# Performance work log

Measured on AMD Instinct MI355X. Metric: run time of the kernel, lower is better.

## Reference

```python
import jax, jax.numpy as jnp
import numpy as np

N, F_IN, F_OUT = 200000, 128, 64
H, DEG = 50000, 32            # num_hyperedges, nodes per hyperedge
E = H * DEG                   # total incidences


def setup_inputs() -> dict:
    key = jax.random.key(0)
    k1, k2, k3, k4 = jax.random.split(key, 4)
    x = jax.random.normal(k1, (N, F_IN), dtype=jnp.float32)
    W = jax.random.normal(k2, (F_OUT, F_IN), dtype=jnp.float32) / np.sqrt(F_IN)
    a = jax.random.normal(k3, (2 * F_OUT,), dtype=jnp.float32) / np.sqrt(2 * F_OUT)
    nodes = jax.random.randint(k4, (E,), 0, N, dtype=jnp.int32)
    edges = jnp.repeat(jnp.arange(H, dtype=jnp.int32), DEG)  # sorted edge ids, DEG nodes each
    hyperedge_index = jnp.stack([nodes, edges])  # (2, E)
    return {"x": x, "W": W, "a": a, "hyperedge_index": hyperedge_index}


def reference(x, W, a, hyperedge_index):
    # h = W x  (Linear without bias, weight stored as (out, in))
    h = x @ W.T                                   # (N, F_OUT)
    nodes = hyperedge_index[0]
    eid = hyperedge_index[1]                      # sorted, groups incidences per hyperedge

    # attention score for ordered pair (j,k): a[:F] . h_j + a[F:] . h_k
    s1 = h @ a[:F_OUT]                            # (N,) left-slot contribution per node
    s2 = h @ a[F_OUT:]                            # (N,) right-slot contribution per node
    s1e = s1[nodes]                               # (E,)
    s2e = s2[nodes]                               # (E,)

    counts = jax.ops.segment_sum(jnp.ones_like(eid), eid, num_segments=H)   # degree per edge
    starts = jnp.cumsum(counts) - counts
    rank = jnp.arange(E, dtype=eid.dtype) - starts[eid]                     # position within edge
    deg_e = counts[eid]
    # sum over pairs j<k of (s1_j + s2_k):
    #   node at rank r appears (deg-1-r) times in left slot, r times in right slot
    w1 = (deg_e - 1 - rank).astype(h.dtype)
    w2 = rank.astype(h.dtype)
    pair_sum = jax.ops.segment_sum(s1e * w1 + s2e * w2, eid, num_segments=H)
    npairs = (counts * (counts - 1)) // 2
    edge_attention = pair_sum / jnp.maximum(npairs, 1).astype(h.dtype)      # mean over pairs
    # all H edges have DEG>=2 nodes by construction, matching torch's non-empty filter
    return h, edge_attention
```

## Files before the change

kernel.cpp:

```cpp
#include <hip/hip_runtime.h>

#define F_IN  128
#define F_OUT 64
#define DEG   32

typedef __attribute__((ext_vector_type(8))) short  short8;
typedef __attribute__((ext_vector_type(4))) float  float4v;

__device__ __forceinline__ unsigned short f2bf(float f) {
    unsigned int u = __builtin_bit_cast(unsigned int, f);
    u += 0x7FFFu + ((u >> 16) & 1u);
    return (unsigned short)(u >> 16);
}

__device__ __forceinline__ short8 cvt8(float4v lo, float4v hi) {
    short8 r;
    r[0] = (short)f2bf(lo[0]); r[1] = (short)f2bf(lo[1]);
    r[2] = (short)f2bf(lo[2]); r[3] = (short)f2bf(lo[3]);
    r[4] = (short)f2bf(hi[0]); r[5] = (short)f2bf(hi[1]);
    r[6] = (short)f2bf(hi[2]); r[7] = (short)f2bf(hi[3]);
    return r;
}

__device__ __forceinline__ short8 load_cvt8(const float* __restrict__ p) {
    const float4v* q = (const float4v*)p;
    return cvt8(q[0], q[1]);
}

__global__ __launch_bounds__(256) void gemm_s12_kernel(
    const float* __restrict__ x, const float* __restrict__ W,
    const float* __restrict__ a, float* __restrict__ h_out,
    float2* __restrict__ s12, int N)
{
    __shared__ short8 wfrag[1024];

    const int tid = threadIdx.x;

#pragma unroll
    for (int i0 = 0; i0 < 1024; i0 += 256) {
        const int i     = i0 + tid;
        const int combo = i >> 6;
        const int sl    = i & 63;
        const int t  = combo >> 2;
        const int ks = combo & 3;
        const int n  = (sl & 15) + 16 * t;
        const int qq = sl >> 4;
        wfrag[i] = load_cvt8(W + n * F_IN + ks * 32 + qq * 8);
    }
    __syncthreads();

    const int lane = tid & 63;
    const int wave = tid >> 6;
    const int row_base = (blockIdx.x * 4 + wave) * 32;
    if (row_base >= N) return;

    const int m = lane & 15;
    const int q = lane >> 4;

    float a1v[4], a2v[4];
#pragma unroll
    for (int t = 0; t < 4; ++t) {
        a1v[t] = a[m + 16 * t];
        a2v[t] = a[F_OUT + m + 16 * t];
    }

#pragma unroll
    for (int s = 0; s < 2; ++s) {
        const int row0 = row_base + s * 16;
        const float* rowp = x + (size_t)(row0 + m) * F_IN + q * 8;

        float4v raw[4][2];
#pragma unroll
        for (int ks = 0; ks < 4; ++ks) {
            const float4v* p = (const float4v*)(rowp + ks * 32);
            raw[ks][0] = p[0];
            raw[ks][1] = p[1];
        }
        short8 afrag[4];
#pragma unroll
        for (int ks = 0; ks < 4; ++ks) afrag[ks] = cvt8(raw[ks][0], raw[ks][1]);

        float4v acc[4];
#pragma unroll
        for (int t = 0; t < 4; ++t) acc[t] = (float4v){0.f, 0.f, 0.f, 0.f};

#pragma unroll
        for (int ks = 0; ks < 4; ++ks) {
#pragma unroll
            for (int t = 0; t < 4; ++t) {
                acc[t] = __builtin_amdgcn_mfma_f32_16x16x32_bf16(
                            afrag[ks], wfrag[(t * 4 + ks) * 64 + lane], acc[t], 0, 0, 0);
            }
        }

        const int rrow = row0 + q * 4;
        float p1[4] = {0.f, 0.f, 0.f, 0.f};
        float p2[4] = {0.f, 0.f, 0.f, 0.f};
#pragma unroll
        for (int t = 0; t < 4; ++t) {
            const int col = m + 16 * t;
#pragma unroll
            for (int r = 0; r < 4; ++r) {
                const float v = acc[t][r];
                h_out[(size_t)(rrow + r) * F_OUT + col] = v;
                p1[r] += v * a1v[t];
                p2[r] += v * a2v[t];
            }
        }
#pragma unroll
        for (int d = 1; d < 16; d <<= 1) {
#pragma unroll
            for (int r = 0; r < 4; ++r) {
                p1[r] += __shfl_xor(p1[r], d);
                p2[r] += __shfl_xor(p2[r], d);
            }
        }
        if (m == 0) {
#pragma unroll
            for (int r = 0; r < 4; ++r)
                s12[rrow + r] = make_float2(p1[r], p2[r]);
        }
    }
}

__global__ __launch_bounds__(256) void edge_att_kernel(
    const int* __restrict__ nodes, const float2* __restrict__ s12,
    float* __restrict__ eatt, int H)
{
    const int t = blockIdx.x * 256 + threadIdx.x;
    const int e = t >> 5;
    const int r = t & 31;
    if (e >= H) return;
    const int node = nodes[(size_t)e * DEG + r];
    const float2 s = s12[node];
    float v = s.x * (float)(DEG - 1 - r) + s.y * (float)r;
#pragma unroll
    for (int d = 1; d < 32; d <<= 1) v += __shfl_xor(v, d);
    if (r == 0) eatt[e] = v * (1.0f / 496.0f);
}

extern "C" void kernel_launch(void* const* d_in, const int* in_sizes, int n_in,
                              void* d_out, int out_size, void* d_ws, size_t ws_size,
                              hipStream_t stream)
{
    const float* x   = (const float*)d_in[0];
    const float* W   = (const float*)d_in[1];
    const float* a   = (const float*)d_in[2];
    const int*   hei = (const int*)d_in[3];

    const int N = in_sizes[0] / F_IN;
    const int E = in_sizes[3] / 2;
    const int H = E / DEG;
    const int* nodes = hei;

    float*  h_out = (float*)d_out;
    float*  eatt  = (float*)d_out + (size_t)N * F_OUT;
    float2* s12   = (float2*)d_ws;

    const int waves  = (N + 31) / 32;
    const int blocks = (waves + 3) / 4;
    gemm_s12_kernel<<<blocks, 256, 0, stream>>>(x, W, a, h_out, s12, N);

    const int eblocks = (E + 255) / 256;
    edge_att_kernel<<<eblocks, 256, 0, stream>>>(nodes, s12, eatt, H);
}
```

Baseline: 191.8 us.

## Swap MFMA operands to get row-contiguous h output and cheaper s12 reduction

Swaps the A/B operands of the bf16 MFMA so each lane holds four consecutive output columns of a single row. h can then be written as float4 vector stores instead of scattered scalar stores, and the attention dot products need only two cross-lane shuffles instead of sixteen per row group. It also adds nontemporal loads and stores for the streaming x, h and nodes traffic. The risk is that nontemporal hints may change cache behavior unpredictably on this hardware.

```diff
diff --git a/kernel.cpp b/kernel.cpp
--- a/kernel.cpp
+++ b/kernel.cpp
@@ -22,11 +22,6 @@
     return r;
 }
 
-__device__ __forceinline__ short8 load_cvt8(const float* __restrict__ p) {
-    const float4v* q = (const float4v*)p;
-    return cvt8(q[0], q[1]);
-}
-
 __global__ __launch_bounds__(256) void gemm_s12_kernel(
     const float* __restrict__ x, const float* __restrict__ W,
     const float* __restrict__ a, float* __restrict__ h_out,
@@ -45,7 +40,8 @@
         const int ks = combo & 3;
         const int n  = (sl & 15) + 16 * t;
         const int qq = sl >> 4;
-        wfrag[i] = load_cvt8(W + n * F_IN + ks * 32 + qq * 8);
+        const float4v* wp = (const float4v*)(W + n * F_IN + ks * 32 + qq * 8);
+        wfrag[i] = cvt8(wp[0], wp[1]);
     }
     __syncthreads();
 
@@ -57,28 +53,22 @@
     const int m = lane & 15;
     const int q = lane >> 4;
 
-    float a1v[4], a2v[4];
-#pragma unroll
-    for (int t = 0; t < 4; ++t) {
-        a1v[t] = a[m + 16 * t];
-        a2v[t] = a[F_OUT + m + 16 * t];
-    }
-
 #pragma unroll
     for (int s = 0; s < 2; ++s) {
         const int row0 = row_base + s * 16;
-        const float* rowp = x + (size_t)(row0 + m) * F_IN + q * 8;
+        const int row  = row0 + m;
+        const float* rowp = x + (size_t)row * F_IN + q * 8;
 
         float4v raw[4][2];
 #pragma unroll
         for (int ks = 0; ks < 4; ++ks) {
             const float4v* p = (const float4v*)(rowp + ks * 32);
-            raw[ks][0] = p[0];
-            raw[ks][1] = p[1];
+            raw[ks][0] = __builtin_nontemporal_load(p);
+            raw[ks][1] = __builtin_nontemporal_load(p + 1);
         }
-        short8 afrag[4];
+        short8 xfrag[4];
 #pragma unroll
-        for (int ks = 0; ks < 4; ++ks) afrag[ks] = cvt8(raw[ks][0], raw[ks][1]);
+        for (int ks = 0; ks < 4; ++ks) xfrag[ks] = cvt8(raw[ks][0], raw[ks][1]);
 
         float4v acc[4];
 #pragma unroll
@@ -89,37 +79,27 @@
 #pragma unroll
             for (int t = 0; t < 4; ++t) {
                 acc[t] = __builtin_amdgcn_mfma_f32_16x16x32_bf16(
-                            afrag[ks], wfrag[(t * 4 + ks) * 64 + lane], acc[t], 0, 0, 0);
+                            wfrag[(t * 4 + ks) * 64 + lane], xfrag[ks], acc[t], 0, 0, 0);
             }
         }
 
-        const int rrow = row0 + q * 4;
-        float p1[4] = {0.f, 0.f, 0.f, 0.f};
-        float p2[4] = {0.f, 0.f, 0.f, 0.f};
+        float4v* hrow = (float4v*)(h_out + (size_t)row * F_OUT);
+        float p1 = 0.f, p2 = 0.f;
 #pragma unroll
         for (int t = 0; t < 4; ++t) {
-            const int col = m + 16 * t;
+            __builtin_nontemporal_store(acc[t], hrow + 4 * t + q);
+            const float4v a1t = *(const float4v*)(a + 16 * t + 4 * q);
+            const float4v a2t = *(const float4v*)(a + F_OUT + 16 * t + 4 * q);
 #pragma unroll
             for (int r = 0; r < 4; ++r) {
-                const float v = acc[t][r];
-                h_out[(size_t)(rrow + r) * F_OUT + col] = v;
-                p1[r] += v * a1v[t];
-                p2[r] += v * a2v[t];
+                p1 += acc[t][r] * a1t[r];
+                p2 += acc[t][r] * a2t[r];
             }
         }
-#pragma unroll
-        for (int d = 1; d < 16; d <<= 1) {
-#pragma unroll
-            for (int r = 0; r < 4; ++r) {
-                p1[r] += __shfl_xor(p1[r], d);
-                p2[r] += __shfl_xor(p2[r], d);
-            }
-        }
-        if (m == 0) {
-#pragma unroll
-            for (int r = 0; r < 4; ++r)
-                s12[rrow + r] = make_float2(p1[r], p2[r]);
-        }
+        p1 += __shfl_xor(p1, 16); p1 += __shfl_xor(p1, 32);
+        p2 += __shfl_xor(p2, 16); p2 += __shfl_xor(p2, 32);
+        if (q == 0)
+            s12[row] = make_float2(p1, p2);
     }
 }
 
@@ -131,7 +111,7 @@
     const int e = t >> 5;
     const int r = t & 31;
     if (e >= H) return;
-    const int node = nodes[(size_t)e * DEG + r];
+    const int node = __builtin_nontemporal_load(nodes + (size_t)e * DEG + r);
     const float2 s = s12[node];
     float v = s.x * (float)(DEG - 1 - r) + s.y * (float)r;
 #pragma unroll
```

Result: no change. 192.7 us (+0.5%).
